# Kernel optimization log

Measured on AMD Instinct MI355X. Metric: run time of the kernel, lower is better.

## Reference

```python
import jax, jax.numpy as jnp
import numpy as np

B, S, T, H, V = 32, 64, 64, 512, 32000


def setup_inputs() -> dict:
    key = jax.random.key(0)
    ks = jax.random.split(key, 14)
    enc = jax.random.normal(ks[0], (B, S, H), jnp.float32)
    h0 = jax.random.normal(ks[1], (1, B, H), jnp.float32)
    # encoder padding mask: at least half of each row valid (avoids all -inf rows)
    src_len = jax.random.randint(ks[2], (B,), S // 2, S + 1)
    enc_mask = (jnp.arange(S)[None, :] < src_len[:, None])
    tgt = jax.random.randint(ks[3], (B, T), 0, V)
    fra_len = jax.random.randint(ks[4], (B,), 1, T + 1).at[0].set(T)
    s = 1.0 / np.sqrt(H)
    emb = jax.random.normal(ks[5], (V, H), jnp.float32) * s
    W_ih = jax.random.uniform(ks[6], (3 * H, H), jnp.float32, -s, s)
    W_hh = jax.random.uniform(ks[7], (3 * H, H), jnp.float32, -s, s)
    b_ih = jax.random.uniform(ks[8], (3 * H,), jnp.float32, -s, s)
    b_hh = jax.random.uniform(ks[9], (3 * H,), jnp.float32, -s, s)
    W_cc = jax.random.uniform(ks[10], (H, 2 * H), jnp.float32, -s, s)
    b_cc = jnp.zeros((H,), jnp.float32)
    W_out = jax.random.uniform(ks[11], (V, H), jnp.float32, -s, s)
    b_out = jnp.zeros((V,), jnp.float32)
    return {"all_encoder_hidden_states": enc, "initial_decoder_hidden_state": h0,
            "encoder_output_mask": enc_mask, "target_input": tgt, "fra_length": fra_len,
            "embedding": emb, "W_ih": W_ih, "W_hh": W_hh, "b_ih": b_ih, "b_hh": b_hh,
            "W_cc": W_cc, "b_cc": b_cc, "W_out": W_out, "b_out": b_out}


def reference(all_encoder_hidden_states, initial_decoder_hidden_state, encoder_output_mask,
              target_input, fra_length, embedding, W_ih, W_hh, b_ih, b_hh,
              W_cc, b_cc, W_out, b_out):
    enc = all_encoder_hidden_states            # [B,S,H]
    mask = encoder_output_mask                 # [B,S] bool
    xs = embedding[target_input].transpose(1, 0, 2)  # [T,B,H]
    ts = jnp.arange(xs.shape[0])

    def step(h, inp):                          # h: [B,H]
        x, t = inp
        gx = x @ W_ih.T + b_ih                 # [B,3H]
        gh = h @ W_hh.T + b_hh
        gxr, gxz, gxn = jnp.split(gx, 3, axis=-1)
        ghr, ghz, ghn = jnp.split(gh, 3, axis=-1)
        r = jax.nn.sigmoid(gxr + ghr)
        z = jax.nn.sigmoid(gxz + ghz)
        n = jnp.tanh(gxn + r * ghn)
        h_new = (1.0 - z) * n + z * h          # torch GRU update
        # Luong dot-product attention
        scores = jnp.einsum('bsh,bh->bs', enc, h_new)
        scores = jnp.where(mask, scores, -jnp.inf)
        alphas = jax.nn.softmax(scores, axis=-1)
        ctx = jnp.einsum('bs,bsh->bh', alphas, enc)
        ho = jnp.tanh(jnp.concatenate([ctx, h_new], axis=-1) @ W_cc.T + b_cc)
        logit = ho @ W_out.T + b_out           # [B,V]
        active = (t < fra_length)[:, None]
        h_next = jnp.where(active, h_new, h)   # freeze finished sequences
        return h_next, logit

    _, logits = jax.lax.scan(step, initial_decoder_hidden_state[0], (xs, ts))
    logits = logits.transpose(1, 0, 2)          # [B,T,V]
    return jax.nn.log_softmax(logits, axis=-1)
```

## Files before the change

kernel.cpp:

```cpp
#include <hip/hip_runtime.h>

static constexpr int Bn = 32, Sn = 64, Tn = 64, Hn = 512, Vn = 32000;
static constexpr int H3 = 1536;

typedef __attribute__((ext_vector_type(8))) short bf16x8;
typedef __attribute__((ext_vector_type(4))) float f32x4;

__device__ __forceinline__ short f2bf(float f) {
    unsigned u = __float_as_uint(f);
    u += 0x7FFFu + ((u >> 16) & 1u);
    return (short)(u >> 16);
}
__device__ __forceinline__ float bf2f(short s) {
    return __uint_as_float(((unsigned)(unsigned short)s) << 16);
}

__device__ __forceinline__ void gload16(const void* g, void* l) {
    __builtin_amdgcn_global_load_lds(
        (const __attribute__((address_space(1))) unsigned int*)g,
        (__attribute__((address_space(3))) unsigned int*)l, 16, 0, 0);
}

__global__ __launch_bounds__(128) void k_gather(const int* __restrict__ tgt,
                                                const float* __restrict__ emb,
                                                short* __restrict__ Xb) {
    int m = blockIdx.x;
    int c = threadIdx.x * 4;
    const float4 v = *(const float4*)(emb + (long)tgt[m] * Hn + c);
    short4 o; o.x = f2bf(v.x); o.y = f2bf(v.y); o.z = f2bf(v.z); o.w = f2bf(v.w);
    *(short4*)(Xb + (long)m * Hn + c) = o;
}

__global__ __launch_bounds__(256) void k_cvt(const float* __restrict__ src, int src_ld, int src_off,
                                             short* __restrict__ dst, long total4) {
    for (long i = (long)blockIdx.x * 256 + threadIdx.x; i < total4; i += (long)gridDim.x * 256) {
        long e = i * 4;
        long r = e >> 9; int c = (int)(e & 511);
        const float4 v = *(const float4*)(src + r * (long)src_ld + src_off + c);
        short4 o; o.x = f2bf(v.x); o.y = f2bf(v.y); o.z = f2bf(v.z); o.w = f2bf(v.w);
        *(short4*)(dst + e) = o;
    }
}

__global__ __launch_bounds__(256) void k_gemm_bf16(const short* __restrict__ A, int lda,
                                                   const short* __restrict__ Bm, int ldb,
                                                   const float* __restrict__ bias,
                                                   float* __restrict__ C, int ldc, int K) {
    __shared__ short lA[4096];
    __shared__ short lB[4096];
    const int tid = threadIdx.x;
    const int row0 = blockIdx.y * 128;
    const int col0 = blockIdx.x * 128;
    const int lane = tid & 63;
    const int w = tid >> 6;
    const int wr = w >> 1, wc = w & 1;
    const int g = lane >> 4, rr = lane & 15;

    f32x4 acc[4][4];
    for (int m = 0; m < 4; ++m)
        for (int n = 0; n < 4; ++n)
            for (int q = 0; q < 4; ++q) acc[m][n][q] = 0.f;

    for (int kk = 0; kk < K; kk += 32) {
        for (int p = 0; p < 2; ++p) {
            int u = p * 256 + tid;
            int kg = u >> 7, r = u & 127;
            gload16(A + (long)(row0 + r) * lda + kk + kg * 8, &lA[u * 8]);
            gload16(Bm + (long)(col0 + r) * ldb + kk + kg * 8, &lB[u * 8]);
        }
        __syncthreads();
        bf16x8 av[4], bv[4];
        for (int m = 0; m < 4; ++m)
            av[m] = *(const bf16x8*)&lA[(g * 128 + wr * 64 + m * 16 + rr) * 8];
        for (int n = 0; n < 4; ++n)
            bv[n] = *(const bf16x8*)&lB[(g * 128 + wc * 64 + n * 16 + rr) * 8];
        for (int m = 0; m < 4; ++m)
            for (int n = 0; n < 4; ++n)
                acc[m][n] = __builtin_amdgcn_mfma_f32_16x16x32_bf16(av[m], bv[n], acc[m][n], 0, 0, 0);
        __syncthreads();
    }

    for (int n = 0; n < 4; ++n) {
        int gc = col0 + wc * 64 + n * 16 + rr;
        float bb = bias ? bias[gc] : 0.f;
        for (int m = 0; m < 4; ++m) {
            int gr = row0 + wr * 64 + m * 16 + g * 4;
            for (int q = 0; q < 4; ++q)
                C[(long)(gr + q) * ldc + gc] = acc[m][n][q] + bb;
        }
    }
}

__global__ __launch_bounds__(256) void k_ho(const short* __restrict__ A1, const short* __restrict__ A2,
                                            const short* __restrict__ B1, const short* __restrict__ B2,
                                            const float* __restrict__ bias, short* __restrict__ C) {
    __shared__ short lA[4096];
    __shared__ short lB[4096];
    const int tid = threadIdx.x;
    const int row0 = blockIdx.y * 128;
    const int col0 = blockIdx.x * 128;
    const int lane = tid & 63;
    const int w = tid >> 6;
    const int wr = w >> 1, wc = w & 1;
    const int g = lane >> 4, rr = lane & 15;

    f32x4 acc[4][4];
    for (int m = 0; m < 4; ++m)
        for (int n = 0; n < 4; ++n)
            for (int q = 0; q < 4; ++q) acc[m][n][q] = 0.f;

    for (int ph = 0; ph < 2; ++ph) {
        const short* A = ph ? A2 : A1;
        const short* Bm = ph ? B2 : B1;
        for (int kk = 0; kk < 512; kk += 32) {
            for (int p = 0; p < 2; ++p) {
                int u = p * 256 + tid;
                int kg = u >> 7, r = u & 127;
                gload16(A + (long)(row0 + r) * 512 + kk + kg * 8, &lA[u * 8]);
                gload16(Bm + (long)(col0 + r) * 512 + kk + kg * 8, &lB[u * 8]);
            }
            __syncthreads();
            bf16x8 av[4], bv[4];
            for (int m = 0; m < 4; ++m)
                av[m] = *(const bf16x8*)&lA[(g * 128 + wr * 64 + m * 16 + rr) * 8];
            for (int n = 0; n < 4; ++n)
                bv[n] = *(const bf16x8*)&lB[(g * 128 + wc * 64 + n * 16 + rr) * 8];
            for (int m = 0; m < 4; ++m)
                for (int n = 0; n < 4; ++n)
                    acc[m][n] = __builtin_amdgcn_mfma_f32_16x16x32_bf16(av[m], bv[n], acc[m][n], 0, 0, 0);
            __syncthreads();
        }
    }

    for (int n = 0; n < 4; ++n) {
        int gc = col0 + wc * 64 + n * 16 + rr;
        float bb = bias[gc];
        for (int m = 0; m < 4; ++m) {
            int gr = row0 + wr * 64 + m * 16 + g * 4;
            for (int q = 0; q < 4; ++q)
                C[(long)(gr + q) * 512 + gc] = f2bf(tanhf(acc[m][n][q] + bb));
        }
    }
}

__device__ __forceinline__ void sig_flag(unsigned* slot, unsigned val) {
    asm volatile("s_waitcnt vmcnt(0)" ::: "memory");
    __syncthreads();
    if (threadIdx.x == 0)
        __hip_atomic_store(slot, val, __ATOMIC_RELAXED, __HIP_MEMORY_SCOPE_AGENT);
}
__device__ __forceinline__ void wait_flags32(const unsigned* base, unsigned need) {
    if (threadIdx.x < 32) {
        while (__hip_atomic_load(base + threadIdx.x * 32, __ATOMIC_RELAXED, __HIP_MEMORY_SCOPE_AGENT) < need)
            __builtin_amdgcn_s_sleep(1);
    }
    __syncthreads();
}

__global__ __launch_bounds__(512, 1) void k_seq(
    const float* __restrict__ GX, const int* __restrict__ fra,
    const float* __restrict__ h0,
    const short* __restrict__ Whh_b, const float* __restrict__ b_hh,
    short* __restrict__ hn_all,
    unsigned long long* __restrict__ hn_pub,
    unsigned* __restrict__ flags)
{
    __shared__ __align__(16) short h_all[Bn * Hn];
    __shared__ float gh_sl[3 * 16 * 32];
    __shared__ int flen[Bn];
    const int bid = blockIdx.x;
    const int tid = threadIdx.x;
    const int wv = tid >> 6, lane = tid & 63;

    bf16x8 afr[16];
    if (wv < 6) {
        const int g = wv >> 1;
        const int row = g * 512 + bid * 16 + (lane & 15);
        #pragma unroll
        for (int k = 0; k < 16; ++k)
            afr[k] = *(const bf16x8*)(Whh_b + (long)row * 512 + k * 32 + (lane >> 4) * 8);
    }
    if (tid < Bn) flen[tid] = fra[tid];
    #pragma unroll
    for (int it = 0; it < 8; ++it) {
        const int idx2 = it * 512 + tid;
        const int b = idx2 >> 7, ci2 = idx2 & 127;
        const int j0 = ci2 * 4;
        const int soff = b * 512 + ((((ci2 >> 1)) ^ (b & 7)) << 3) + (ci2 & 1) * 4;
        const float4 v = *(const float4*)(h0 + b * 512 + j0);
        unsigned long long pk = (unsigned long long)(unsigned short)f2bf(v.x)
                              | ((unsigned long long)(unsigned short)f2bf(v.y) << 16)
                              | ((unsigned long long)(unsigned short)f2bf(v.z) << 32)
                              | ((unsigned long long)(unsigned short)f2bf(v.w) << 48);
        *(unsigned long long*)&h_all[soff] = pk;
    }

    const int eb = tid >> 4, jj = tid & 15;
    float h_carry = h0[eb * 512 + bid * 16 + jj];
    const int flen_e = fra[eb];

    for (int t = 0; t < Tn; ++t) {
        const long base = (long)(eb * Tn + t) * H3 + bid * 16 + jj;
        const float gxr = GX[base];
        const float gxz = GX[base + 512];
        const float gxn = GX[base + 1024];
        if (t >= 1) {
            wait_flags32(flags, (unsigned)t);
            const unsigned long long* src = hn_pub + ((t - 1) & 1) * 4096;
            #pragma unroll
            for (int it = 0; it < 8; ++it) {
                const int idx2 = it * 512 + tid;
                const int b = idx2 >> 7, ci2 = idx2 & 127;
                if (t - 1 < flen[b]) {
                    const int soff = b * 512 + ((((ci2 >> 1)) ^ (b & 7)) << 3) + (ci2 & 1) * 4;
                    *(unsigned long long*)&h_all[soff] =
                        __hip_atomic_load(src + idx2, __ATOMIC_RELAXED, __HIP_MEMORY_SCOPE_AGENT);
                }
            }
        }
        __syncthreads();
        if (wv < 6) {
            const int g = wv >> 1, n = wv & 1;
            const int bq = n * 16 + (lane & 15);
            f32x4 a0 = {0.f, 0.f, 0.f, 0.f}, a1 = {0.f, 0.f, 0.f, 0.f};
            #pragma unroll
            for (int k = 0; k < 8; ++k) {
                const int c0 = k * 4 + (lane >> 4);
                const int c1 = (k + 8) * 4 + (lane >> 4);
                bf16x8 b0 = *(const bf16x8*)&h_all[bq * 512 + ((c0 ^ (bq & 7)) << 3)];
                bf16x8 b1 = *(const bf16x8*)&h_all[bq * 512 + ((c1 ^ (bq & 7)) << 3)];
                a0 = __builtin_amdgcn_mfma_f32_16x16x32_bf16(afr[k], b0, a0, 0, 0, 0);
                a1 = __builtin_amdgcn_mfma_f32_16x16x32_bf16(afr[k + 8], b1, a1, 0, 0, 0);
            }
            const int r0 = (lane >> 4) * 4;
            #pragma unroll
            for (int q = 0; q < 4; ++q)
                gh_sl[g * 512 + (r0 + q) * 32 + bq] = a0[q] + a1[q];
        }
        __syncthreads();
        {
            const int j = bid * 16 + jj;
            const float ghr = gh_sl[jj * 32 + eb]          + b_hh[j];
            const float ghz = gh_sl[512 + jj * 32 + eb]    + b_hh[512 + j];
            const float ghn = gh_sl[1024 + jj * 32 + eb]   + b_hh[1024 + j];
            const float r = 1.f / (1.f + expf(-(gxr + ghr)));
            const float z = 1.f / (1.f + expf(-(gxz + ghz)));
            const float nn = tanhf(gxn + r * ghn);
            const float hv = (1.f - z) * nn + z * h_carry;
            h_carry = (t < flen_e) ? hv : h_carry;
            const short hb = f2bf(hv);
            int w32 = (int)(unsigned short)hb;
            int n1 = __shfl_down(w32, 1);
            int n2 = __shfl_down(w32, 2);
            int n3 = __shfl_down(w32, 3);
            if ((jj & 3) == 0) {
                unsigned long long pk = (unsigned long long)(unsigned)(w32 | (n1 << 16))
                                      | ((unsigned long long)(unsigned)(n2 | (n3 << 16)) << 32);
                __hip_atomic_store(hn_pub + (t & 1) * 4096 + eb * 128 + bid * 4 + (jj >> 2), pk,
                                   __ATOMIC_RELAXED, __HIP_MEMORY_SCOPE_AGENT);
            }
            sig_flag(flags + bid * 32, (unsigned)(t + 1));
            hn_all[(long)(eb * Tn + t) * Hn + bid * 16 + jj] = hb;
        }
    }
}

__global__ __launch_bounds__(512, 1) void k_attn(
    const float* __restrict__ enc, const short* __restrict__ hn_all,
    const void* __restrict__ maskp, short* __restrict__ ctx_b)
{
    __shared__ __align__(16) short encl[64 * 536];
    __shared__ __align__(16) short hnlbuf[64 * 536];
    __shared__ __align__(16) float scl[64 * 64];
    __shared__ __align__(16) short albc[64 * 72];
    const int b = blockIdx.x;
    const int tid = threadIdx.x;
    const int wv = tid >> 6, lane = tid & 63;
    const int g = lane >> 4, rr = lane & 15;

    const unsigned w0 = ((const unsigned*)maskp)[0];
    const int mmode = (w0 == 1u) ? 0 : (w0 == 0x3F800000u ? 2 : 1);

    {
        const float* encb = enc + (long)b * (Sn * Hn);
        #pragma unroll
        for (int it = 0; it < 16; ++it) {
            int e = (it * 512 + tid) * 4;
            float4 v = *(const float4*)(encb + e);
            int s = e >> 9, k = e & 511;
            short4 o; o.x = f2bf(v.x); o.y = f2bf(v.y); o.z = f2bf(v.z); o.w = f2bf(v.w);
            *(short4*)(encl + s * 536 + k) = o;
        }
    }
    {
        const short* hb = hn_all + (long)b * (Tn * Hn);
        #pragma unroll
        for (int it = 0; it < 8; ++it) {
            int u = it * 512 + tid;
            int t = u >> 6, k8 = (u & 63) * 8;
            *(int4*)(hnlbuf + t * 536 + k8) = *(const int4*)(hb + t * 512 + k8);
        }
    }
    __syncthreads();

    for (int i = 0; i < 2; ++i) {
        const int id = wv * 2 + i;
        const int tt = id >> 2, ss = id & 3;
        f32x4 a0 = {0.f, 0.f, 0.f, 0.f}, a1 = {0.f, 0.f, 0.f, 0.f};
        #pragma unroll
        for (int k = 0; k < 8; ++k) {
            bf16x8 av0 = *(const bf16x8*)&hnlbuf[(tt * 16 + rr) * 536 + k * 32 + g * 8];
            bf16x8 bv0 = *(const bf16x8*)&encl[(ss * 16 + rr) * 536 + k * 32 + g * 8];
            bf16x8 av1 = *(const bf16x8*)&hnlbuf[(tt * 16 + rr) * 536 + (k + 8) * 32 + g * 8];
            bf16x8 bv1 = *(const bf16x8*)&encl[(ss * 16 + rr) * 536 + (k + 8) * 32 + g * 8];
            a0 = __builtin_amdgcn_mfma_f32_16x16x32_bf16(av0, bv0, a0, 0, 0, 0);
            a1 = __builtin_amdgcn_mfma_f32_16x16x32_bf16(av1, bv1, a1, 0, 0, 0);
        }
        #pragma unroll
        for (int q = 0; q < 4; ++q)
            scl[(tt * 16 + g * 4 + q) * 64 + ss * 16 + rr] = a0[q] + a1[q];
    }
    __syncthreads();

    {
        const int t = wv * 8 + (lane >> 3);
        const int sub = lane & 7;
        float v[8];
        #pragma unroll
        for (int e = 0; e < 8; ++e) {
            const int s = sub * 8 + e;
            bool mv;
            if (mmode == 0)      mv = ((const int*)maskp)[b * Sn + s] != 0;
            else if (mmode == 1) mv = ((const unsigned char*)maskp)[b * Sn + s] != 0;
            else                 mv = ((const float*)maskp)[b * Sn + s] != 0.f;
            v[e] = mv ? scl[t * 64 + s] : -__builtin_inff();
        }
        float mx = v[0];
        #pragma unroll
        for (int e = 1; e < 8; ++e) mx = fmaxf(mx, v[e]);
        mx = fmaxf(mx, __shfl_xor(mx, 1));
        mx = fmaxf(mx, __shfl_xor(mx, 2));
        mx = fmaxf(mx, __shfl_xor(mx, 4));
        float su = 0.f;
        float ev[8];
        #pragma unroll
        for (int e = 0; e < 8; ++e) { ev[e] = __expf(v[e] - mx); su += ev[e]; }
        su += __shfl_xor(su, 1);
        su += __shfl_xor(su, 2);
        su += __shfl_xor(su, 4);
        const float inv = 1.f / su;
        bf16x8 o;
        #pragma unroll
        for (int e = 0; e < 8; ++e) o[e] = f2bf(ev[e] * inv);
        *(bf16x8*)&albc[t * 72 + sub * 8] = o;
    }
    {
        short* enct = hnlbuf;
        const int j = tid;
        #pragma unroll
        for (int c = 0; c < 8; ++c) {
            bf16x8 tmp;
            #pragma unroll
            for (int e = 0; e < 8; ++e) tmp[e] = encl[(c * 8 + e) * 536 + j];
            *(bf16x8*)&enct[j * 64 + ((c ^ (j & 7)) * 8)] = tmp;
        }
    }
    __syncthreads();

    {
        const short* enct = hnlbuf;
        for (int i = 0; i < 16; ++i) {
            const int id = wv * 16 + i;
            const int tt = id >> 5, jt = id & 31;
            const int jr = jt * 16 + rr;
            f32x4 acc = {0.f, 0.f, 0.f, 0.f};
            #pragma unroll
            for (int kk = 0; kk < 2; ++kk) {
                bf16x8 av = *(const bf16x8*)&albc[(tt * 16 + rr) * 72 + kk * 32 + g * 8];
                const int c = kk * 4 + g;
                bf16x8 bv = *(const bf16x8*)&enct[jr * 64 + ((c ^ (jr & 7)) * 8)];
                acc = __builtin_amdgcn_mfma_f32_16x16x32_bf16(av, bv, acc, 0, 0, 0);
            }
            #pragma unroll
            for (int q = 0; q < 4; ++q) {
                const int t = tt * 16 + g * 4 + q;
                ctx_b[(long)(b * Tn + t) * Hn + jr] = f2bf(acc[q]);
            }
        }
    }
}

__global__ __launch_bounds__(256) void k_logsoftmax(float* __restrict__ out) {
    const long row = blockIdx.x;
    float* p = out + row * (long)Vn;
    const int tid = threadIdx.x;
    __shared__ float redm[4];
    __shared__ float reds[4];

    float mx = -__builtin_inff(), sm = 0.f;
    for (int i = tid; i < Vn / 4; i += 256) {
        float4 v = *(const float4*)(p + i * 4);
        float ml = fmaxf(fmaxf(v.x, v.y), fmaxf(v.z, v.w));
        float nm = fmaxf(mx, ml);
        sm = sm * __expf(mx - nm) + __expf(v.x - nm) + __expf(v.y - nm) + __expf(v.z - nm) + __expf(v.w - nm);
        mx = nm;
    }
    for (int o = 1; o < 64; o <<= 1) {
        float omx = __shfl_xor(mx, o), osm = __shfl_xor(sm, o);
        float nm = fmaxf(mx, omx);
        sm = sm * __expf(mx - nm) + osm * __expf(omx - nm);
        mx = nm;
    }
    if ((tid & 63) == 0) { redm[tid >> 6] = mx; reds[tid >> 6] = sm; }
    __syncthreads();
    float gmx = fmaxf(fmaxf(redm[0], redm[1]), fmaxf(redm[2], redm[3]));
    float gsm = reds[0] * __expf(redm[0] - gmx) + reds[1] * __expf(redm[1] - gmx)
              + reds[2] * __expf(redm[2] - gmx) + reds[3] * __expf(redm[3] - gmx);
    const float lse = gmx + logf(gsm);

    for (int i = tid; i < Vn / 4; i += 256) {
        float4 v = *(const float4*)(p + i * 4);
        v.x -= lse; v.y -= lse; v.z -= lse; v.w -= lse;
        *(float4*)(p + i * 4) = v;
    }
}

extern "C" void kernel_launch(void* const* d_in, const int* in_sizes, int n_in,
                              void* d_out, int out_size, void* d_ws, size_t ws_size,
                              hipStream_t stream) {
    const float* enc   = (const float*)d_in[0];
    const float* h0    = (const float*)d_in[1];
    const void*  maskp = d_in[2];
    const int*   tgt   = (const int*)d_in[3];
    const int*   fra   = (const int*)d_in[4];
    const float* emb   = (const float*)d_in[5];
    const float* W_ih  = (const float*)d_in[6];
    const float* W_hh  = (const float*)d_in[7];
    const float* b_ih  = (const float*)d_in[8];
    const float* b_hh  = (const float*)d_in[9];
    const float* W_cc  = (const float*)d_in[10];
    const float* b_cc  = (const float*)d_in[11];
    const float* W_out = (const float*)d_in[12];
    const float* b_out = (const float*)d_in[13];
    float* out = (float*)d_out;

    char* ws = (char*)d_ws;
    float*    GX      = (float*)ws;   ws += (long)2048 * 1536 * 4;
    short*    Xb      = (short*)ws;   ws += (long)2048 * 512 * 2;
    short*    Wih_b   = (short*)ws;   ws += (long)1536 * 512 * 2;
    short*    Wout_b  = (short*)ws;   ws += (long)32000 * 512 * 2;
    short*    Whh_b   = (short*)ws;   ws += (long)1536 * 512 * 2;
    short*    Wc1_b   = (short*)ws;   ws += (long)512 * 512 * 2;
    short*    Wcc2_b  = (short*)ws;   ws += (long)512 * 512 * 2;
    short*    ho_b    = (short*)ws;   ws += (long)2048 * 512 * 2;
    short*    hn_all  = (short*)ws;   ws += (long)2048 * 512 * 2;
    short*    ctx_b   = (short*)ws;   ws += (long)2048 * 512 * 2;
    unsigned long long* hn_pub = (unsigned long long*)ws; ws += (long)2 * 4096 * 8;
    unsigned* flags   = (unsigned*)ws; ws += 1024 * 4;

    k_gather<<<2048, 128, 0, stream>>>(tgt, emb, Xb);
    k_cvt<<<768, 256, 0, stream>>>(W_ih, 512, 0, Wih_b, (long)1536 * 512 / 4);
    k_cvt<<<4096, 256, 0, stream>>>(W_out, 512, 0, Wout_b, (long)32000 * 512 / 4);
    k_cvt<<<768, 256, 0, stream>>>(W_hh, 512, 0, Whh_b, (long)1536 * 512 / 4);
    k_cvt<<<256, 256, 0, stream>>>(W_cc, 1024, 0, Wc1_b, (long)512 * 512 / 4);
    k_cvt<<<256, 256, 0, stream>>>(W_cc, 1024, 512, Wcc2_b, (long)512 * 512 / 4);

    k_gemm_bf16<<<dim3(12, 16), 256, 0, stream>>>(Xb, 512, Wih_b, 512, b_ih, GX, 1536, 512);

    hipMemsetAsync(flags, 0, 1024 * 4, stream);
    k_seq<<<32, 512, 0, stream>>>(GX, fra, h0, Whh_b, b_hh, hn_all, hn_pub, flags);

    k_attn<<<32, 512, 0, stream>>>(enc, hn_all, maskp, ctx_b);

    k_ho<<<dim3(4, 16), 256, 0, stream>>>(ctx_b, hn_all, Wc1_b, Wcc2_b, b_cc, ho_b);

    k_gemm_bf16<<<dim3(250, 16), 256, 0, stream>>>(ho_b, 512, Wout_b, 512, b_out, out, 32000, 512);

    k_logsoftmax<<<2048, 256, 0, stream>>>(out);
}
```

Measured before the change: 689.1 us.

## Fuse logsoftmax stats into logits GEMM, merge weight casts, per-producer flag waits

The logits GEMM epilogue now computes per-tile row max and sum-exp, writing them to a stats buffer. A light k_sub kernel combines the 250 partials per row and subtracts the LSE, which removes the full extra read pass of the old logsoftmax. Small weight conversions are merged into one launch. In the recurrent kernel each thread now spins only on the flag of the block that produced its slice, and always loads the published carried state instead of gating on sequence length. It also uses fast exp for the gates.

New measurement: 716.3 us. 4.0% more time.

```diff
diff --git a/kernel.cpp b/kernel.cpp
--- a/kernel.cpp
+++ b/kernel.cpp
@@ -31,15 +31,31 @@
     *(short4*)(Xb + (long)m * Hn + c) = o;
 }
 
-__global__ __launch_bounds__(256) void k_cvt(const float* __restrict__ src, int src_ld, int src_off,
-                                             short* __restrict__ dst, long total4) {
-    for (long i = (long)blockIdx.x * 256 + threadIdx.x; i < total4; i += (long)gridDim.x * 256) {
-        long e = i * 4;
-        long r = e >> 9; int c = (int)(e & 511);
-        const float4 v = *(const float4*)(src + r * (long)src_ld + src_off + c);
-        short4 o; o.x = f2bf(v.x); o.y = f2bf(v.y); o.z = f2bf(v.z); o.w = f2bf(v.w);
-        *(short4*)(dst + e) = o;
-    }
+__global__ __launch_bounds__(256) void k_cvt_flat(const float* __restrict__ src,
+                                                  short* __restrict__ dst, long n4) {
+    long i = (long)blockIdx.x * 256 + threadIdx.x;
+    if (i >= n4) return;
+    const float4 v = *(const float4*)(src + i * 4);
+    short4 o; o.x = f2bf(v.x); o.y = f2bf(v.y); o.z = f2bf(v.z); o.w = f2bf(v.w);
+    *(short4*)(dst + i * 4) = o;
+}
+
+__global__ __launch_bounds__(256) void k_cvtW(const float* __restrict__ W_ih,
+                                              const float* __restrict__ W_hh,
+                                              const float* __restrict__ W_cc,
+                                              short* __restrict__ Wih_b, short* __restrict__ Whh_b,
+                                              short* __restrict__ Wc1_b, short* __restrict__ Wc2_b) {
+    long u = (long)blockIdx.x * 256 + threadIdx.x;
+    const float* src; short* dst;
+    if (u < 196608)       { long e = u * 4;            src = W_ih + e; dst = Wih_b + e; }
+    else if (u < 393216)  { long e = (u - 196608) * 4; src = W_hh + e; dst = Whh_b + e; }
+    else if (u < 458752)  { long e = (u - 393216) * 4; long r = e >> 9; int c = (int)(e & 511);
+                            src = W_cc + r * 1024 + c;       dst = Wc1_b + e; }
+    else                  { long e = (u - 458752) * 4; long r = e >> 9; int c = (int)(e & 511);
+                            src = W_cc + r * 1024 + 512 + c; dst = Wc2_b + e; }
+    const float4 v = *(const float4*)src;
+    short4 o; o.x = f2bf(v.x); o.y = f2bf(v.y); o.z = f2bf(v.z); o.w = f2bf(v.w);
+    *(short4*)dst = o;
 }
 
 __global__ __launch_bounds__(256) void k_gemm_bf16(const short* __restrict__ A, int lda,
@@ -91,6 +107,126 @@
     }
 }
 
+__global__ __launch_bounds__(256) void k_gemm_logits(const short* __restrict__ A,
+                                                     const short* __restrict__ Bm,
+                                                     const float* __restrict__ bias,
+                                                     float* __restrict__ C,
+                                                     float* __restrict__ stats) {
+    __shared__ short lA[4096];
+    __shared__ short lB[4096];
+    __shared__ float sml[128][2];
+    __shared__ float ssl[128][2];
+    const int tid = threadIdx.x;
+    const int row0 = blockIdx.y * 128;
+    const int col0 = blockIdx.x * 128;
+    const int lane = tid & 63;
+    const int w = tid >> 6;
+    const int wr = w >> 1, wc = w & 1;
+    const int g = lane >> 4, rr = lane & 15;
+
+    f32x4 acc[4][4];
+    for (int m = 0; m < 4; ++m)
+        for (int n = 0; n < 4; ++n)
+            for (int q = 0; q < 4; ++q) acc[m][n][q] = 0.f;
+
+    for (int kk = 0; kk < 512; kk += 32) {
+        for (int p = 0; p < 2; ++p) {
+            int u = p * 256 + tid;
+            int kg = u >> 7, r = u & 127;
+            gload16(A + (long)(row0 + r) * 512 + kk + kg * 8, &lA[u * 8]);
+            gload16(Bm + (long)(col0 + r) * 512 + kk + kg * 8, &lB[u * 8]);
+        }
+        __syncthreads();
+        bf16x8 av[4], bv[4];
+        for (int m = 0; m < 4; ++m)
+            av[m] = *(const bf16x8*)&lA[(g * 128 + wr * 64 + m * 16 + rr) * 8];
+        for (int n = 0; n < 4; ++n)
+            bv[n] = *(const bf16x8*)&lB[(g * 128 + wc * 64 + n * 16 + rr) * 8];
+        for (int m = 0; m < 4; ++m)
+            for (int n = 0; n < 4; ++n)
+                acc[m][n] = __builtin_amdgcn_mfma_f32_16x16x32_bf16(av[m], bv[n], acc[m][n], 0, 0, 0);
+        __syncthreads();
+    }
+
+    float bb[4];
+    #pragma unroll
+    for (int n = 0; n < 4; ++n) bb[n] = bias[col0 + wc * 64 + n * 16 + rr];
+
+    #pragma unroll
+    for (int n = 0; n < 4; ++n) {
+        int gc = col0 + wc * 64 + n * 16 + rr;
+        #pragma unroll
+        for (int m = 0; m < 4; ++m) {
+            int gr = row0 + wr * 64 + m * 16 + g * 4;
+            #pragma unroll
+            for (int q = 0; q < 4; ++q)
+                C[(long)(gr + q) * Vn + gc] = acc[m][n][q] + bb[n];
+        }
+    }
+    #pragma unroll
+    for (int m = 0; m < 4; ++m) {
+        #pragma unroll
+        for (int q = 0; q < 4; ++q) {
+            float mx = acc[m][0][q] + bb[0];
+            mx = fmaxf(mx, acc[m][1][q] + bb[1]);
+            mx = fmaxf(mx, acc[m][2][q] + bb[2]);
+            mx = fmaxf(mx, acc[m][3][q] + bb[3]);
+            mx = fmaxf(mx, __shfl_xor(mx, 1));
+            mx = fmaxf(mx, __shfl_xor(mx, 2));
+            mx = fmaxf(mx, __shfl_xor(mx, 4));
+            mx = fmaxf(mx, __shfl_xor(mx, 8));
+            float s = __expf(acc[m][0][q] + bb[0] - mx) + __expf(acc[m][1][q] + bb[1] - mx)
+                    + __expf(acc[m][2][q] + bb[2] - mx) + __expf(acc[m][3][q] + bb[3] - mx);
+            s += __shfl_xor(s, 1);
+            s += __shfl_xor(s, 2);
+            s += __shfl_xor(s, 4);
+            s += __shfl_xor(s, 8);
+            if (rr == 0) {
+                const int r = wr * 64 + m * 16 + g * 4 + q;
+                sml[r][wc] = mx; ssl[r][wc] = s;
+            }
+        }
+    }
+    __syncthreads();
+    if (tid < 128) {
+        const float m0 = sml[tid][0], m1 = sml[tid][1];
+        const float mm = fmaxf(m0, m1);
+        const float ss = ssl[tid][0] * __expf(m0 - mm) + ssl[tid][1] * __expf(m1 - mm);
+        float2* sp = (float2*)stats;
+        sp[(long)(row0 + tid) * 256 + blockIdx.x] = make_float2(mm, ss);
+    }
+}
+
+__global__ __launch_bounds__(256) void k_sub(float* __restrict__ out, const float* __restrict__ stats) {
+    const long row = blockIdx.x;
+    const int tid = threadIdx.x;
+    __shared__ float lse_s;
+    if (tid < 64) {
+        float m = -__builtin_inff(), s = 0.f;
+        for (int tc = tid; tc < 250; tc += 64) {
+            const float2 p = ((const float2*)stats)[row * 256 + tc];
+            const float nm = fmaxf(m, p.x);
+            s = s * __expf(m - nm) + p.y * __expf(p.x - nm);
+            m = nm;
+        }
+        for (int o = 1; o < 64; o <<= 1) {
+            const float om = __shfl_xor(m, o), os = __shfl_xor(s, o);
+            const float nm = fmaxf(m, om);
+            s = s * __expf(m - nm) + os * __expf(om - nm);
+            m = nm;
+        }
+        if (tid == 0) lse_s = m + logf(s);
+    }
+    __syncthreads();
+    const float lse = lse_s;
+    float* p = out + row * (long)Vn;
+    for (int i = tid; i < Vn / 4; i += 256) {
+        float4 v = *(const float4*)(p + i * 4);
+        v.x -= lse; v.y -= lse; v.z -= lse; v.w -= lse;
+        *(float4*)(p + i * 4) = v;
+    }
+}
+
 __global__ __launch_bounds__(256) void k_ho(const short* __restrict__ A1, const short* __restrict__ A2,
                                             const short* __restrict__ B1, const short* __restrict__ B2,
                                             const float* __restrict__ bias, short* __restrict__ C) {
@@ -149,13 +285,6 @@
     if (threadIdx.x == 0)
         __hip_atomic_store(slot, val, __ATOMIC_RELAXED, __HIP_MEMORY_SCOPE_AGENT);
 }
-__device__ __forceinline__ void wait_flags32(const unsigned* base, unsigned need) {
-    if (threadIdx.x < 32) {
-        while (__hip_atomic_load(base + threadIdx.x * 32, __ATOMIC_RELAXED, __HIP_MEMORY_SCOPE_AGENT) < need)
-            __builtin_amdgcn_s_sleep(1);
-    }
-    __syncthreads();
-}
 
 __global__ __launch_bounds__(512, 1) void k_seq(
     const float* __restrict__ GX, const int* __restrict__ fra,
@@ -167,7 +296,6 @@
 {
     __shared__ __align__(16) short h_all[Bn * Hn];
     __shared__ float gh_sl[3 * 16 * 32];
-    __shared__ int flen[Bn];
     const int bid = blockIdx.x;
     const int tid = threadIdx.x;
     const int wv = tid >> 6, lane = tid & 63;
@@ -180,7 +308,6 @@
         for (int k = 0; k < 16; ++k)
             afr[k] = *(const bf16x8*)(Whh_b + (long)row * 512 + k * 32 + (lane >> 4) * 8);
     }
-    if (tid < Bn) flen[tid] = fra[tid];
     #pragma unroll
     for (int it = 0; it < 8; ++it) {
         const int idx2 = it * 512 + tid;
@@ -199,23 +326,26 @@
     float h_carry = h0[eb * 512 + bid * 16 + jj];
     const int flen_e = fra[eb];
 
+    const int ci2s = wv * 16 + (lane & 15);
+    const unsigned* fp = flags + (ci2s >> 2) * 32;
+    const int bbase = lane >> 4;
+
     for (int t = 0; t < Tn; ++t) {
         const long base = (long)(eb * Tn + t) * H3 + bid * 16 + jj;
         const float gxr = GX[base];
         const float gxz = GX[base + 512];
         const float gxn = GX[base + 1024];
         if (t >= 1) {
-            wait_flags32(flags, (unsigned)t);
+            while (__hip_atomic_load(fp, __ATOMIC_RELAXED, __HIP_MEMORY_SCOPE_AGENT) < (unsigned)t)
+                __builtin_amdgcn_s_sleep(1);
             const unsigned long long* src = hn_pub + ((t - 1) & 1) * 4096;
             #pragma unroll
             for (int it = 0; it < 8; ++it) {
-                const int idx2 = it * 512 + tid;
-                const int b = idx2 >> 7, ci2 = idx2 & 127;
-                if (t - 1 < flen[b]) {
-                    const int soff = b * 512 + ((((ci2 >> 1)) ^ (b & 7)) << 3) + (ci2 & 1) * 4;
-                    *(unsigned long long*)&h_all[soff] =
-                        __hip_atomic_load(src + idx2, __ATOMIC_RELAXED, __HIP_MEMORY_SCOPE_AGENT);
-                }
+                const int b = bbase + it * 4;
+                const unsigned long long v =
+                    __hip_atomic_load(src + b * 128 + ci2s, __ATOMIC_RELAXED, __HIP_MEMORY_SCOPE_AGENT);
+                const int soff = b * 512 + ((((ci2s >> 1)) ^ (b & 7)) << 3) + (ci2s & 1) * 4;
+                *(unsigned long long*)&h_all[soff] = v;
             }
         }
         __syncthreads();
@@ -243,13 +373,12 @@
             const float ghr = gh_sl[jj * 32 + eb]          + b_hh[j];
             const float ghz = gh_sl[512 + jj * 32 + eb]    + b_hh[512 + j];
             const float ghn = gh_sl[1024 + jj * 32 + eb]   + b_hh[1024 + j];
-            const float r = 1.f / (1.f + expf(-(gxr + ghr)));
-            const float z = 1.f / (1.f + expf(-(gxz + ghz)));
+            const float r = 1.f / (1.f + __expf(-(gxr + ghr)));
+            const float z = 1.f / (1.f + __expf(-(gxz + ghz)));
             const float nn = tanhf(gxn + r * ghn);
             const float hv = (1.f - z) * nn + z * h_carry;
             h_carry = (t < flen_e) ? hv : h_carry;
-            const short hb = f2bf(hv);
-            int w32 = (int)(unsigned short)hb;
+            int w32 = (int)(unsigned short)f2bf(h_carry);
             int n1 = __shfl_down(w32, 1);
             int n2 = __shfl_down(w32, 2);
             int n3 = __shfl_down(w32, 3);
@@ -260,7 +389,7 @@
                                    __ATOMIC_RELAXED, __HIP_MEMORY_SCOPE_AGENT);
             }
             sig_flag(flags + bid * 32, (unsigned)(t + 1));
-            hn_all[(long)(eb * Tn + t) * Hn + bid * 16 + jj] = hb;
+            hn_all[(long)(eb * Tn + t) * Hn + bid * 16 + jj] = f2bf(hv);
         }
     }
 }
@@ -387,41 +516,6 @@
                 ctx_b[(long)(b * Tn + t) * Hn + jr] = f2bf(acc[q]);
             }
         }
-    }
-}
-
-__global__ __launch_bounds__(256) void k_logsoftmax(float* __restrict__ out) {
-    const long row = blockIdx.x;
-    float* p = out + row * (long)Vn;
-    const int tid = threadIdx.x;
-    __shared__ float redm[4];
-    __shared__ float reds[4];
-
-    float mx = -__builtin_inff(), sm = 0.f;
-    for (int i = tid; i < Vn / 4; i += 256) {
-        float4 v = *(const float4*)(p + i * 4);
-        float ml = fmaxf(fmaxf(v.x, v.y), fmaxf(v.z, v.w));
-        float nm = fmaxf(mx, ml);
-        sm = sm * __expf(mx - nm) + __expf(v.x - nm) + __expf(v.y - nm) + __expf(v.z - nm) + __expf(v.w - nm);
-        mx = nm;
-    }
-    for (int o = 1; o < 64; o <<= 1) {
-        float omx = __shfl_xor(mx, o), osm = __shfl_xor(sm, o);
-        float nm = fmaxf(mx, omx);
-        sm = sm * __expf(mx - nm) + osm * __expf(omx - nm);
-        mx = nm;
-    }
-    if ((tid & 63) == 0) { redm[tid >> 6] = mx; reds[tid >> 6] = sm; }
-    __syncthreads();
-    float gmx = fmaxf(fmaxf(redm[0], redm[1]), fmaxf(redm[2], redm[3]));
-    float gsm = reds[0] * __expf(redm[0] - gmx) + reds[1] * __expf(redm[1] - gmx)
-              + reds[2] * __expf(redm[2] - gmx) + reds[3] * __expf(redm[3] - gmx);
-    const float lse = gmx + logf(gsm);
-
-    for (int i = tid; i < Vn / 4; i += 256) {
-        float4 v = *(const float4*)(p + i * 4);
-        v.x -= lse; v.y -= lse; v.z -= lse; v.w -= lse;
-        *(float4*)(p + i * 4) = v;
     }
 }
 
@@ -455,26 +549,24 @@
     short*    ho_b    = (short*)ws;   ws += (long)2048 * 512 * 2;
     short*    hn_all  = (short*)ws;   ws += (long)2048 * 512 * 2;
     short*    ctx_b   = (short*)ws;   ws += (long)2048 * 512 * 2;
+    float*    stats   = (float*)ws;   ws += (long)2048 * 256 * 2 * 4;
     unsigned long long* hn_pub = (unsigned long long*)ws; ws += (long)2 * 4096 * 8;
     unsigned* flags   = (unsigned*)ws; ws += 1024 * 4;
 
+    hipMemsetAsync(flags, 0, 1024 * 4, stream);
     k_gather<<<2048, 128, 0, stream>>>(tgt, emb, Xb);
-    k_cvt<<<768, 256, 0, stream>>>(W_ih, 512, 0, Wih_b, (long)1536 * 512 / 4);
-    k_cvt<<<4096, 256, 0, stream>>>(W_out, 512, 0, Wout_b, (long)32000 * 512 / 4);
-    k_cvt<<<768, 256, 0, stream>>>(W_hh, 512, 0, Whh_b, (long)1536 * 512 / 4);
-    k_cvt<<<256, 256, 0, stream>>>(W_cc, 1024, 0, Wc1_b, (long)512 * 512 / 4);
-    k_cvt<<<256, 256, 0, stream>>>(W_cc, 1024, 512, Wcc2_b, (long)512 * 512 / 4);
+    k_cvtW<<<2048, 256, 0, stream>>>(W_ih, W_hh, W_cc, Wih_b, Whh_b, Wc1_b, Wcc2_b);
+    k_cvt_flat<<<16000, 256, 0, stream>>>(W_out, Wout_b, (long)32000 * 512 / 4);
 
     k_gemm_bf16<<<dim3(12, 16), 256, 0, stream>>>(Xb, 512, Wih_b, 512, b_ih, GX, 1536, 512);
 
-    hipMemsetAsync(flags, 0, 1024 * 4, stream);
     k_seq<<<32, 512, 0, stream>>>(GX, fra, h0, Whh_b, b_hh, hn_all, hn_pub, flags);
 
     k_attn<<<32, 512, 0, stream>>>(enc, hn_all, maskp, ctx_b);
 
     k_ho<<<dim3(4, 16), 256, 0, stream>>>(ctx_b, hn_all, Wc1_b, Wcc2_b, b_cc, ho_b);
 
-    k_gemm_bf16<<<dim3(250, 16), 256, 0, stream>>>(ho_b, 512, Wout_b, 512, b_out, out, 32000, 512);
-
-    k_logsoftmax<<<2048, 256, 0, stream>>>(out);
-}
+    k_gemm_logits<<<dim3(250, 16), 256, 0, stream>>>(ho_b, Wout_b, b_out, out, stats);
+
+    k_sub<<<2048, 256, 0, stream>>>(out, stats);
+}
```
